# Kernel optimization log

Measured on AMD Instinct MI355X. Metric: run time of the kernel, lower is better.

## Reference

```python
import jax, jax.numpy as jnp
import numpy as np

LOG_CLAMP = -100.0  # torch.nn.BCELoss clamps log terms at -100


def setup_inputs() -> dict:
    key = jax.random.key(0)
    k1, k2 = jax.random.split(key)
    shape = (64, 8, 65536, 1)  # [B, C, H, W]
    vertical_pred = jax.random.uniform(k1, shape, dtype=jnp.float32)
    vertical_true = jax.random.uniform(k2, shape, dtype=jnp.float32)
    return {"vertical_pred": vertical_pred, "vertical_true": vertical_true}


def reference(vertical_pred, vertical_true):
    # Only the first width column is used: [B, C, H]
    p = vertical_pred[..., 0]
    t = vertical_true[..., 0]
    log_p = jnp.clip(jnp.log(p), LOG_CLAMP)
    log_1mp = jnp.clip(jnp.log1p(-p), LOG_CLAMP)
    bce = -(t * log_p + (1.0 - t) * log_1mp)           # [B, C, H]
    per_bc = jnp.mean(bce, axis=-1)                     # mean over H per (b, c)
    loss = jnp.sum(per_bc) / vertical_pred.shape[0]     # sum over b,c then / B
    return loss
```

## Files before the change

kernel.cpp:

```cpp
#include <hip/hip_runtime.h>


#define LOG_CLAMP -100.0f

__global__ __launch_bounds__(256) void vertical_loss_kernel(
    const float4* __restrict__ p4,
    const float4* __restrict__ t4,
    float* __restrict__ out,
    int n4, float scale)
{
    int tid    = blockIdx.x * blockDim.x + threadIdx.x;
    int stride = gridDim.x * blockDim.x;

    float sum = 0.0f;
    for (int i = tid; i < n4; i += stride) {
        float4 p = p4[i];
        float4 t = t4[i];

        float lpx = fmaxf(__logf(p.x), LOG_CLAMP);
        float lpy = fmaxf(__logf(p.y), LOG_CLAMP);
        float lpz = fmaxf(__logf(p.z), LOG_CLAMP);
        float lpw = fmaxf(__logf(p.w), LOG_CLAMP);

        float lqx = fmaxf(__logf(1.0f - p.x), LOG_CLAMP);
        float lqy = fmaxf(__logf(1.0f - p.y), LOG_CLAMP);
        float lqz = fmaxf(__logf(1.0f - p.z), LOG_CLAMP);
        float lqw = fmaxf(__logf(1.0f - p.w), LOG_CLAMP);

        sum += t.x * lpx + (1.0f - t.x) * lqx;
        sum += t.y * lpy + (1.0f - t.y) * lqy;
        sum += t.z * lpz + (1.0f - t.z) * lqz;
        sum += t.w * lpw + (1.0f - t.w) * lqw;
    }

    #pragma unroll
    for (int off = 32; off > 0; off >>= 1)
        sum += __shfl_down(sum, off, 64);

    __shared__ float wsum[4];
    int wave = threadIdx.x >> 6;
    int lane = threadIdx.x & 63;
    if (lane == 0) wsum[wave] = sum;
    __syncthreads();

    if (threadIdx.x == 0) {
        float s = wsum[0] + wsum[1] + wsum[2] + wsum[3];
        atomicAdd(out, -s * scale);
    }
}

extern "C" void kernel_launch(void* const* d_in, const int* in_sizes, int n_in,
                              void* d_out, int out_size, void* d_ws, size_t ws_size,
                              hipStream_t stream) {
    const float4* pred = (const float4*)d_in[0];
    const float4* true_ = (const float4*)d_in[1];
    float* out = (float*)d_out;

    int n = in_sizes[0];
    int n4 = n / 4;
    float scale = 1.0f / (65536.0f * 64.0f);

    hipMemsetAsync(d_out, 0, sizeof(float), stream);

    int blocks = 2048;
    vertical_loss_kernel<<<blocks, 256, 0, stream>>>(pred, true_, out, n4, scale);
}
```

Measured before the change: 281.3 us.

## Use contiguous per-block chunks with register double-buffered loads and log2 algebra

Each block now walks a contiguous chunk instead of a grid-stride loop. The next group of four float4 loads per input is issued before computing on the current group, with sched_barriers keeping the loads ahead of the math so memory latency overlaps compute. The math moves to log2 with the ln2 factor folded into the final scale, and is rewritten as sum(lq) + t*(lp-lq) to save multiplies. The cost is extra register pressure from the prefetched operands and a fallback path for sizes that do not divide evenly.

```diff
diff --git a/kernel.cpp b/kernel.cpp
--- a/kernel.cpp
+++ b/kernel.cpp
@@ -1,37 +1,68 @@
 #include <hip/hip_runtime.h>
 
 
-#define LOG_CLAMP -100.0f
+#define LOG2_CLAMP -144.26950408889634f
+
+__device__ __forceinline__ void bce4_acc(const float4& p, const float4& t,
+                                         float& sq, float& sd) {
+    float lp, lq;
+    lp = fmaxf(__log2f(p.x), LOG2_CLAMP);
+    lq = fmaxf(__log2f(1.0f - p.x), LOG2_CLAMP);
+    sq += lq; sd = __builtin_fmaf(t.x, lp - lq, sd);
+    lp = fmaxf(__log2f(p.y), LOG2_CLAMP);
+    lq = fmaxf(__log2f(1.0f - p.y), LOG2_CLAMP);
+    sq += lq; sd = __builtin_fmaf(t.y, lp - lq, sd);
+    lp = fmaxf(__log2f(p.z), LOG2_CLAMP);
+    lq = fmaxf(__log2f(1.0f - p.z), LOG2_CLAMP);
+    sq += lq; sd = __builtin_fmaf(t.z, lp - lq, sd);
+    lp = fmaxf(__log2f(p.w), LOG2_CLAMP);
+    lq = fmaxf(__log2f(1.0f - p.w), LOG2_CLAMP);
+    sq += lq; sd = __builtin_fmaf(t.w, lp - lq, sd);
+}
 
 __global__ __launch_bounds__(256) void vertical_loss_kernel(
     const float4* __restrict__ p4,
     const float4* __restrict__ t4,
     float* __restrict__ out,
-    int n4, float scale)
+    int n4, float final_scale)
 {
-    int tid    = blockIdx.x * blockDim.x + threadIdx.x;
-    int stride = gridDim.x * blockDim.x;
+    float sq = 0.0f, sd = 0.0f;
 
-    float sum = 0.0f;
-    for (int i = tid; i < n4; i += stride) {
-        float4 p = p4[i];
-        float4 t = t4[i];
+    const int chunk = n4 / (int)gridDim.x;
+    const int steps = chunk / (int)blockDim.x;
 
-        float lpx = fmaxf(__logf(p.x), LOG_CLAMP);
-        float lpy = fmaxf(__logf(p.y), LOG_CLAMP);
-        float lpz = fmaxf(__logf(p.z), LOG_CLAMP);
-        float lpw = fmaxf(__logf(p.w), LOG_CLAMP);
+    if ((chunk % (int)blockDim.x) == 0 && (steps & 3) == 0 && steps >= 8) {
+        const int stp = (int)blockDim.x;
+        int i = (int)blockIdx.x * chunk + (int)threadIdx.x;
 
-        float lqx = fmaxf(__logf(1.0f - p.x), LOG_CLAMP);
-        float lqy = fmaxf(__logf(1.0f - p.y), LOG_CLAMP);
-        float lqz = fmaxf(__logf(1.0f - p.z), LOG_CLAMP);
-        float lqw = fmaxf(__logf(1.0f - p.w), LOG_CLAMP);
+        float4 P0 = p4[i], P1 = p4[i + stp], P2 = p4[i + 2 * stp], P3 = p4[i + 3 * stp];
+        float4 T0 = t4[i], T1 = t4[i + stp], T2 = t4[i + 2 * stp], T3 = t4[i + 3 * stp];
 
-        sum += t.x * lpx + (1.0f - t.x) * lqx;
-        sum += t.y * lpy + (1.0f - t.y) * lqy;
-        sum += t.z * lpz + (1.0f - t.z) * lqz;
-        sum += t.w * lpw + (1.0f - t.w) * lqw;
+        const int groups = steps >> 2;
+        for (int g = 1; g < groups; ++g) {
+            i += 4 * stp;
+            __builtin_amdgcn_sched_barrier(0);
+            float4 Q0 = p4[i], Q1 = p4[i + stp], Q2 = p4[i + 2 * stp], Q3 = p4[i + 3 * stp];
+            float4 U0 = t4[i], U1 = t4[i + stp], U2 = t4[i + 2 * stp], U3 = t4[i + 3 * stp];
+            __builtin_amdgcn_sched_barrier(0);
+            bce4_acc(P0, T0, sq, sd);
+            bce4_acc(P1, T1, sq, sd);
+            bce4_acc(P2, T2, sq, sd);
+            bce4_acc(P3, T3, sq, sd);
+            P0 = Q0; P1 = Q1; P2 = Q2; P3 = Q3;
+            T0 = U0; T1 = U1; T2 = U2; T3 = U3;
+        }
+        bce4_acc(P0, T0, sq, sd);
+        bce4_acc(P1, T1, sq, sd);
+        bce4_acc(P2, T2, sq, sd);
+        bce4_acc(P3, T3, sq, sd);
+    } else {
+        for (int i = (int)blockIdx.x * (int)blockDim.x + (int)threadIdx.x;
+             i < n4; i += (int)gridDim.x * (int)blockDim.x)
+            bce4_acc(p4[i], t4[i], sq, sd);
     }
+
+    float sum = sq + sd;
 
     #pragma unroll
     for (int off = 32; off > 0; off >>= 1)
@@ -45,23 +76,23 @@
 
     if (threadIdx.x == 0) {
         float s = wsum[0] + wsum[1] + wsum[2] + wsum[3];
-        atomicAdd(out, -s * scale);
+        atomicAdd(out, s * final_scale);
     }
 }
 
 extern "C" void kernel_launch(void* const* d_in, const int* in_sizes, int n_in,
                               void* d_out, int out_size, void* d_ws, size_t ws_size,
                               hipStream_t stream) {
-    const float4* pred = (const float4*)d_in[0];
+    const float4* pred  = (const float4*)d_in[0];
     const float4* true_ = (const float4*)d_in[1];
     float* out = (float*)d_out;
 
-    int n = in_sizes[0];
+    int n  = in_sizes[0];
     int n4 = n / 4;
-    float scale = 1.0f / (65536.0f * 64.0f);
+    float final_scale = -0.69314718055994531f / (65536.0f * 64.0f);
 
     hipMemsetAsync(d_out, 0, sizeof(float), stream);
 
     int blocks = 2048;
-    vertical_loss_kernel<<<blocks, 256, 0, stream>>>(pred, true_, out, n4, scale);
+    vertical_loss_kernel<<<blocks, 256, 0, stream>>>(pred, true_, out, n4, final_scale);
 }
```

Result: no change. 278.4 us (-1.0%).
